# Performance work log

Hardware: AMD Instinct MI355X
Metric: run time of the kernel (lower is better)

The kernel has to match this reference:

```python
import math
import jax, jax.numpy as jnp
import numpy as np

B, T, C, H, DQK, DV = 2, 2048, 1024, 16, 64, 64


def setup_inputs() -> dict:
    key = jax.random.key(0)
    ks = jax.random.split(key, 5)
    x = jax.random.normal(ks[0], (B, T, C), dtype=jnp.float32)
    # randw: randn(*d) / sqrt(d[-1])
    w_q = jax.random.normal(ks[1], (H, DQK, C), dtype=jnp.float32) / math.sqrt(C)
    w_k = jax.random.normal(ks[2], (H, DQK, C), dtype=jnp.float32) / math.sqrt(C)
    w_v = jax.random.normal(ks[3], (H, DV, C), dtype=jnp.float32) / math.sqrt(C)
    w_o = jax.random.normal(ks[4], (DV * H, C), dtype=jnp.float32) / math.sqrt(C)
    return {"x": x, "w_q": w_q, "w_k": w_k, "w_v": w_v, "w_o": w_o}


def reference(x, w_q, w_k, w_v, w_o):
    # Full-sequence causal forward (bs_q.first == 0, nb == T): caches are
    # fully written in one shot, so they reduce to the plain projections.
    n, t, c = x.shape
    q = jnp.einsum('ntc,hdc->nhtd', x, w_q)
    k = jnp.einsum('ntc,hdc->nhtd', x, w_k)
    v = jnp.einsum('ntc,hdc->nhtd', x, w_v)
    scale = 1.0 / math.sqrt(w_q.shape[1])
    a = jnp.einsum('nhtd,nhsd->nhts', q, k) * scale  # [n,h,t,s]
    causal = jnp.arange(t)[:, None] < jnp.arange(t)[None, :]  # True above diag
    a = jnp.where(causal[None, None, :, :], -jnp.inf, a)
    a = jax.nn.softmax(a, axis=3)
    y = jnp.einsum('nhts,nhsd->nthd', a, v).reshape(n, t, -1)  # [n,t,h*dv]
    return y @ w_o  # cache_y, [n,t,c]
```

## Files before the change

### kernel.cpp

```cpp
#include <hip/hip_runtime.h>


typedef short bf16x4 __attribute__((ext_vector_type(4)));
typedef short bf16x8 __attribute__((ext_vector_type(8)));
typedef float f32x4 __attribute__((ext_vector_type(4)));

#define MFMA_BF16 __builtin_amdgcn_mfma_f32_16x16x32_bf16

#define QSCALE 0.18033688011112042f

__device__ __forceinline__ unsigned short f2bf(float f) {
    union { float f; unsigned u; } un; un.f = f;
    unsigned r = un.u + 0x7fffu + ((un.u >> 16) & 1u);
    return (unsigned short)(r >> 16);
}
__device__ __forceinline__ unsigned pk2(float a, float b) {
    return (unsigned)f2bf(a) | ((unsigned)f2bf(b) << 16);
}
__device__ __forceinline__ unsigned pk2t(float a, float b) {
    union { float f; unsigned u; } ua, ub; ua.f = a; ub.f = b;
    return __builtin_amdgcn_perm(ub.u, ua.u, 0x07060302u);
}
__device__ __forceinline__ void gload16(const void* g, void* l) {
    __builtin_amdgcn_global_load_lds(
        (const __attribute__((address_space(1))) unsigned int*)g,
        (__attribute__((address_space(3))) unsigned int*)l, 16, 0, 0);
}

__global__ __launch_bounds__(256) void prep(
    const float* __restrict__ x, const float* __restrict__ wq,
    const float* __restrict__ wk, const float* __restrict__ wv,
    const float* __restrict__ wo,
    unsigned short* __restrict__ x16, unsigned short* __restrict__ wq16,
    unsigned short* __restrict__ wk16, unsigned short* __restrict__ wv16,
    unsigned short* __restrict__ wot)
{
    const int bid = blockIdx.x;
    if (bid < 3584) {
        const float* s; unsigned short* d; int off;
        if (bid < 2048)      { s = x;  d = x16;  off = bid * 2048; }
        else if (bid < 2560) { s = wq; d = wq16; off = (bid - 2048) * 2048; }
        else if (bid < 3072) { s = wk; d = wk16; off = (bid - 2560) * 2048; }
        else                 { s = wv; d = wv16; off = (bid - 3072) * 2048; }
        int i = off + threadIdx.x * 8;
        float4 f0 = *(const float4*)&s[i], f1 = *(const float4*)&s[i + 4];
        uint4 o;
        o.x = pk2(f0.x, f0.y); o.y = pk2(f0.z, f0.w);
        o.z = pk2(f1.x, f1.y); o.w = pk2(f1.z, f1.w);
        *(uint4*)&d[i] = o;
    } else {
        __shared__ unsigned short t[64 * 72];
        const int b2 = bid - 3584;
        const int k0 = (b2 & 15) << 6, n0 = (b2 >> 4) << 6;
        const int r = threadIdx.x >> 2, cg = (threadIdx.x & 3) << 4;
        const float* src = &wo[(k0 + r) * 1024 + n0 + cg];
        #pragma unroll
        for (int j = 0; j < 16; j += 4) {
            float4 f = *(const float4*)&src[j];
            t[(cg + j + 0) * 72 + r] = f2bf(f.x);
            t[(cg + j + 1) * 72 + r] = f2bf(f.y);
            t[(cg + j + 2) * 72 + r] = f2bf(f.z);
            t[(cg + j + 3) * 72 + r] = f2bf(f.w);
        }
        __syncthreads();
        unsigned short* dst = &wot[(n0 + r) * 1024 + k0 + cg];
        unsigned short* tr = &t[r * 72 + cg];
        unsigned v[16];
        #pragma unroll
        for (int j = 0; j < 16; ++j) v[j] = tr[j];
        uint4 o0, o1;
        o0.x = v[0] | (v[1] << 16);   o0.y = v[2] | (v[3] << 16);
        o0.z = v[4] | (v[5] << 16);   o0.w = v[6] | (v[7] << 16);
        o1.x = v[8] | (v[9] << 16);   o1.y = v[10] | (v[11] << 16);
        o1.z = v[12] | (v[13] << 16); o1.w = v[14] | (v[15] << 16);
        *(uint4*)&dst[0] = o0;
        *(uint4*)&dst[8] = o1;
    }
}

__device__ __forceinline__ void gemm_body(
    const unsigned short* __restrict__ A, const unsigned short* __restrict__ Bm,
    void* __restrict__ C, int m0, int n0, int mode, int ldc, float sc)
{
    __shared__ unsigned short sa[2][128 * 32];
    __shared__ unsigned short sb[2][128 * 32];
    const int tid = threadIdx.x, wave = tid >> 6, lane = tid & 63;
    const int l15 = lane & 15, l4 = lane >> 4;
    const int wm = (wave >> 1) << 6, wn = (wave & 1) << 6;

    const int r16 = lane >> 2;
    const int gcol = (((lane & 3) ^ ((r16 >> 1) & 3)) << 3);
    const int rcol = (l4 ^ ((l15 >> 1) & 3)) << 3;
    const unsigned short* Ag0 = &A[(size_t)(m0 + wave * 16 + r16) * 1024 + gcol];
    const unsigned short* Ag1 = Ag0 + (size_t)64 * 1024;
    const unsigned short* Bg0 = &Bm[(size_t)(n0 + wave * 16 + r16) * 1024 + gcol];
    const unsigned short* Bg1 = Bg0 + (size_t)64 * 1024;
    const int lb0 = (wave * 16) * 32;
    const int lb1 = (64 + wave * 16) * 32;

    gload16(Ag0, &sa[0][lb0]);
    gload16(Ag1, &sa[0][lb1]);
    gload16(Bg0, &sb[0][lb0]);
    gload16(Bg1, &sb[0][lb1]);
    __syncthreads();

    f32x4 acc[4][4] = {};

    #pragma unroll
    for (int kk = 0; kk < 32; ++kk) {
        const int cur = kk & 1;
        if (kk < 31) {
            const int off = (kk + 1) * 32;
            const int nxt = 1 - cur;
            gload16(Ag0 + off, &sa[nxt][lb0]);
            gload16(Ag1 + off, &sa[nxt][lb1]);
            gload16(Bg0 + off, &sb[nxt][lb0]);
            gload16(Bg1 + off, &sb[nxt][lb1]);
        }
        bf16x8 af[4], bf4[4];
        #pragma unroll
        for (int i = 0; i < 4; ++i)
            af[i] = *(const bf16x8*)&sa[cur][(wm + i * 16 + l15) * 32 + rcol];
        #pragma unroll
        for (int j = 0; j < 4; ++j)
            bf4[j] = *(const bf16x8*)&sb[cur][(wn + j * 16 + l15) * 32 + rcol];
        #pragma unroll
        for (int i = 0; i < 4; ++i)
            #pragma unroll
            for (int j = 0; j < 4; ++j)
                acc[i][j] = MFMA_BF16(af[i], bf4[j], acc[i][j], 0, 0, 0);
        __syncthreads();
    }

    #pragma unroll
    for (int i = 0; i < 4; ++i)
        #pragma unroll
        for (int j = 0; j < 4; ++j)
            #pragma unroll
            for (int r = 0; r < 4; ++r) {
                int row = m0 + wm + i * 16 + l4 * 4 + r;
                int col = n0 + wn + j * 16 + l15;
                float val = acc[i][j][r];
                if (mode == 0) {
                    int nb = row >> 11, t = row & 2047;
                    int hh = col >> 6, dd = col & 63;
                    ((unsigned short*)C)[(((nb << 4) + hh) * 2048 + t) * 64 + dd] =
                        f2bf(val * sc);
                } else if (mode == 1) {
                    ((float*)C)[(size_t)row * ldc + col] = val;
                } else {
                    int s = col & 31;
                    int cp = (col & ~31) | (((s >> 2) & 3) << 3)
                                         | (((s >> 4) & 1) << 2) | (s & 3);
                    ((unsigned short*)C)[(size_t)row * ldc + cp] = f2bf(val);
                }
            }
}

__global__ __launch_bounds__(256) void proj(
    const unsigned short* __restrict__ x16,
    const unsigned short* __restrict__ wq16,
    const unsigned short* __restrict__ wk16,
    const unsigned short* __restrict__ wv16,
    unsigned short* __restrict__ qbuf,
    unsigned short* __restrict__ kbuf,
    unsigned short* __restrict__ vtb)
{
    const int bid = blockIdx.x;
    if (bid < 512) {
        int m0 = (bid & 31) << 7;
        int n0g = (bid >> 5) << 7;
        if (n0g < 1024)
            gemm_body(x16, wq16, qbuf, m0, n0g, 0, 0, QSCALE);
        else
            gemm_body(x16, wk16, kbuf, m0, n0g - 1024, 0, 0, 1.0f);
    } else {
        int v = bid - 512;
        gemm_body(wv16, x16, vtb, (v & 7) << 7, (v >> 3) << 7, 2, 4096, 1.0f);
    }
}

__global__ __launch_bounds__(256) void outp(
    const unsigned short* __restrict__ ybuf,
    const unsigned short* __restrict__ wot,
    float* __restrict__ out)
{
    const int bid = blockIdx.x;
    gemm_body(ybuf, wot, out, (bid & 31) << 7, (bid >> 5) << 7, 1, 1024, 1.0f);
}

__global__ __launch_bounds__(512, 2) void attn(
    const unsigned short* __restrict__ q,
    const unsigned short* __restrict__ k,
    const unsigned short* __restrict__ vt,
    unsigned short* __restrict__ y)
{
    __shared__ unsigned short sk[2][2][64 * 64];
    __shared__ unsigned short sv[2][2][64 * 64];
    const int tid = threadIdx.x, wave = tid >> 6, lane = tid & 63;
    const int ws = wave & 3, wk2 = wave >> 2;
    const int l15 = lane & 15, l4 = lane >> 4;
    const int bid = blockIdx.x;
    const int pr = bid >> 5;
    const int bh = bid & 31;
    const int nb = bh >> 4, hh = bh & 15;
    const size_t base = (size_t)bh << 17;

    const int lrow = lane >> 3;
    const int gch = ((lane & 7) ^ lrow) << 3;
    const int row = wave * 8 + lrow;
    const unsigned short* kg = &k[base + (size_t)row * 64 + gch];
    const unsigned short* vg = &vt[(size_t)((hh << 6) + row) * 4096 + (nb << 11) + gch];
    const int lb = (wave * 8) * 64;

    const int rch0 = ((0 + l4) ^ (l15 & 7)) << 3;
    const int rch1 = ((4 + l4) ^ (l15 & 7)) << 3;

    float* mrg = (float*)&sk[0][0][0];
    float* lsr = (float*)&sv[0][0][0];
    const int mslot = (ws << 6) + lane;
    const int mb = mslot << 5;

    auto process = [&](const int t) {
        const int q0 = t << 7;
        bf16x8 qf[2][2];
        #pragma unroll
        for (int g = 0; g < 2; ++g)
            #pragma unroll
            for (int ks = 0; ks < 2; ++ks)
                qf[g][ks] = *(const bf16x8*)
                    &q[base + (size_t)(q0 + (g << 6) + ws * 16 + l15) * 64 + ks * 32 + l4 * 8];

        float l_sum[2] = {0.f, 0.f};
        f32x4 acc[2][4] = {};
        const int nsup = t + 1;

        auto stage_pair = [&](const int sbuf, const int p) {
            gload16(kg + ((size_t)p << 13),        &sk[sbuf][0][lb]);
            gload16(kg + ((size_t)p << 13) + 4096, &sk[sbuf][1][lb]);
            gload16(vg + (p << 7),      &sv[sbuf][0][lb]);
            gload16(vg + (p << 7) + 64, &sv[sbuf][1][lb]);
        };

        stage_pair(0, 0);
        __syncthreads();

        auto sstep = [&](const int cur, const int p) {
            if (p + 1 < nsup) stage_pair(cur ^ 1, p + 1);
            const int st = 2 * p + wk2;
            const unsigned short* skc = &sk[cur][wk2][0];
            const unsigned short* svc = &sv[cur][wk2][0];

            f32x4 s_acc[2][4] = {};
            #pragma unroll
            for (int ns = 0; ns < 4; ++ns) {
                bf16x8 kf0 = *(const bf16x8*)&skc[(ns * 16 + l15) * 64 + rch0];
                bf16x8 kf1 = *(const bf16x8*)&skc[(ns * 16 + l15) * 64 + rch1];
                s_acc[0][ns] = MFMA_BF16(kf0, qf[0][0], s_acc[0][ns], 0, 0, 0);
                s_acc[0][ns] = MFMA_BF16(kf1, qf[0][1], s_acc[0][ns], 0, 0, 0);
                s_acc[1][ns] = MFMA_BF16(kf0, qf[1][0], s_acc[1][ns], 0, 0, 0);
                s_acc[1][ns] = MFMA_BF16(kf1, qf[1][1], s_acc[1][ns], 0, 0, 0);
            }

            if (p == nsup - 1) {
                const int sb = st << 6;
                #pragma unroll
                for (int g = 0; g < 2; ++g) {
                    const int qlg = q0 + (g << 6) + ws * 16 + l15;
                    #pragma unroll
                    for (int ns = 0; ns < 4; ++ns)
                        #pragma unroll
                        for (int r = 0; r < 4; ++r)
                            if (sb + ns * 16 + l4 * 4 + r > qlg) s_acc[g][ns][r] = -1e30f;
                }
            }

            float pe[2][4][4];
            #pragma unroll
            for (int g = 0; g < 2; ++g)
                #pragma unroll
                for (int ns = 0; ns < 4; ++ns) {
                    #pragma unroll
                    for (int r = 0; r < 4; ++r) pe[g][ns][r] = exp2f(s_acc[g][ns][r]);
                    l_sum[g] += (pe[g][ns][0] + pe[g][ns][1]) + (pe[g][ns][2] + pe[g][ns][3]);
                }

            #pragma unroll
            for (int ks = 0; ks < 2; ++ks) {
                bf16x8 pf0, pf1;
                {
                    uint4 pw;
                    pw.x = pk2t(pe[0][2 * ks][0], pe[0][2 * ks][1]);
                    pw.y = pk2t(pe[0][2 * ks][2], pe[0][2 * ks][3]);
                    pw.z = pk2t(pe[0][2 * ks + 1][0], pe[0][2 * ks + 1][1]);
                    pw.w = pk2t(pe[0][2 * ks + 1][2], pe[0][2 * ks + 1][3]);
                    pf0 = *(bf16x8*)&pw;
                }
                {
                    uint4 pw;
                    pw.x = pk2t(pe[1][2 * ks][0], pe[1][2 * ks][1]);
                    pw.y = pk2t(pe[1][2 * ks][2], pe[1][2 * ks][3]);
                    pw.z = pk2t(pe[1][2 * ks + 1][0], pe[1][2 * ks + 1][1]);
                    pw.w = pk2t(pe[1][2 * ks + 1][2], pe[1][2 * ks + 1][3]);
                    pf1 = *(bf16x8*)&pw;
                }
                const int rch = ks ? rch1 : rch0;
                #pragma unroll
                for (int ds = 0; ds < 4; ++ds) {
                    bf16x8 vf = *(const bf16x8*)&svc[(ds * 16 + l15) * 64 + rch];
                    acc[0][ds] = MFMA_BF16(vf, pf0, acc[0][ds], 0, 0, 0);
                    acc[1][ds] = MFMA_BF16(vf, pf1, acc[1][ds], 0, 0, 0);
                }
            }
            __syncthreads();
        };

        int p = 0;
        for (; p + 2 <= nsup; p += 2) { sstep(0, p); sstep(1, p + 1); }
        if (p < nsup) sstep(0, p);

        if (wk2 == 1) {
            #pragma unroll
            for (int g = 0; g < 2; ++g)
                #pragma unroll
                for (int ds = 0; ds < 4; ++ds) {
                    const int c = g * 4 + ds;
                    *(f32x4*)&mrg[mb + ((c ^ (lane & 7)) << 2)] = acc[g][ds];
                }
            lsr[(mslot << 1) + 0] = l_sum[0];
            lsr[(mslot << 1) + 1] = l_sum[1];
        }
        __syncthreads();
        if (wk2 == 0) {
            #pragma unroll
            for (int g = 0; g < 2; ++g)
                #pragma unroll
                for (int ds = 0; ds < 4; ++ds) {
                    const int c = g * 4 + ds;
                    acc[g][ds] += *(const f32x4*)&mrg[mb + ((c ^ (lane & 7)) << 2)];
                }
            l_sum[0] += lsr[(mslot << 1) + 0];
            l_sum[1] += lsr[(mslot << 1) + 1];

            #pragma unroll
            for (int g = 0; g < 2; ++g) {
                float ls = l_sum[g];
                ls += __shfl_xor(ls, 16);
                ls += __shfl_xor(ls, 32);
                const float rl = __builtin_amdgcn_rcpf(ls);

                const size_t rowbase =
                    ((size_t)((nb << 11) + q0 + (g << 6) + ws * 16 + l15) << 10) + (hh << 6) + l4 * 4;
                #pragma unroll
                for (int ds = 0; ds < 4; ++ds) {
                    uint2 o;
                    o.x = pk2(acc[g][ds][0] * rl, acc[g][ds][1] * rl);
                    o.y = pk2(acc[g][ds][2] * rl, acc[g][ds][3] * rl);
                    *(uint2*)&y[rowbase + ds * 16] = o;
                }
            }
        }
        __syncthreads();
    };

    process(15 - pr);
    process(pr);
}

extern "C" void kernel_launch(void* const* d_in, const int* in_sizes, int n_in,
                              void* d_out, int out_size, void* d_ws, size_t ws_size,
                              hipStream_t stream) {
    const float* x  = (const float*)d_in[0];
    const float* wq = (const float*)d_in[1];
    const float* wk = (const float*)d_in[2];
    const float* wv = (const float*)d_in[3];
    const float* wo = (const float*)d_in[4];
    float* out = (float*)d_out;

    const size_t M1 = 1u << 20;
    unsigned short* x16  = (unsigned short*)d_ws;
    unsigned short* wq16 = x16 + 4 * M1;
    unsigned short* wk16 = wq16 + M1;
    unsigned short* wv16 = wk16 + M1;
    unsigned short* wot  = wv16 + M1;
    unsigned short* qbuf = wot + M1;
    unsigned short* kbuf = qbuf + 4 * M1;
    unsigned short* vtb  = kbuf + 4 * M1;
    unsigned short* ybuf = vtb + 4 * M1;

    dim3 blk(256);
    prep<<<3840, blk, 0, stream>>>(x, wq, wk, wv, wo, x16, wq16, wk16, wv16, wot);
    proj<<<768, blk, 0, stream>>>(x16, wq16, wk16, wv16, qbuf, kbuf, vtb);
    attn<<<256, dim3(512), 0, stream>>>(qbuf, kbuf, vtb, ybuf);
    outp<<<256, blk, 0, stream>>>(ybuf, wot, out);
}
```

Measured before the change: 169.2 us.

## Split-K the output projection with atomics and raise MFMA priority in attention

The output projection now runs as 512 blocks, each covering half of the K dimension, so the 256 CUs are better filled. Partial sums go to the output through float atomic adds, and the prep kernel gains 512 extra blocks that zero the output first. Separately, the attention kernel raises wave priority around its MFMA sections with s_setprio. The cost is atomic traffic on the output plus an extra zeroing write pass, and float atomic ordering may make results nondeterministic.

Result: slower. 199.7 us (+18.0%).

```diff
diff --git a/kernel.cpp b/kernel.cpp
--- a/kernel.cpp
+++ b/kernel.cpp
@@ -33,7 +33,7 @@
     const float* __restrict__ wo,
     unsigned short* __restrict__ x16, unsigned short* __restrict__ wq16,
     unsigned short* __restrict__ wk16, unsigned short* __restrict__ wv16,
-    unsigned short* __restrict__ wot)
+    unsigned short* __restrict__ wot, float* __restrict__ outz)
 {
     const int bid = blockIdx.x;
     if (bid < 3584) {
@@ -48,7 +48,7 @@
         o.x = pk2(f0.x, f0.y); o.y = pk2(f0.z, f0.w);
         o.z = pk2(f1.x, f1.y); o.w = pk2(f1.z, f1.w);
         *(uint4*)&d[i] = o;
-    } else {
+    } else if (bid < 3840) {
         __shared__ unsigned short t[64 * 72];
         const int b2 = bid - 3584;
         const int k0 = (b2 & 15) << 6, n0 = (b2 >> 4) << 6;
@@ -75,12 +75,18 @@
         o1.z = v[12] | (v[13] << 16); o1.w = v[14] | (v[15] << 16);
         *(uint4*)&dst[0] = o0;
         *(uint4*)&dst[8] = o1;
+    } else {
+        float4 z = make_float4(0.f, 0.f, 0.f, 0.f);
+        float* d = &outz[(size_t)(bid - 3840) * 8192 + threadIdx.x * 4];
+        #pragma unroll
+        for (int j = 0; j < 8; ++j) *(float4*)&d[j * 1024] = z;
     }
 }
 
+template<int MODE, int KCNT>
 __device__ __forceinline__ void gemm_body(
     const unsigned short* __restrict__ A, const unsigned short* __restrict__ Bm,
-    void* __restrict__ C, int m0, int n0, int mode, int ldc, float sc)
+    void* __restrict__ C, int m0, int n0, int ldc, float sc, int kbase)
 {
     __shared__ unsigned short sa[2][128 * 32];
     __shared__ unsigned short sb[2][128 * 32];
@@ -91,9 +97,9 @@
     const int r16 = lane >> 2;
     const int gcol = (((lane & 3) ^ ((r16 >> 1) & 3)) << 3);
     const int rcol = (l4 ^ ((l15 >> 1) & 3)) << 3;
-    const unsigned short* Ag0 = &A[(size_t)(m0 + wave * 16 + r16) * 1024 + gcol];
+    const unsigned short* Ag0 = &A[(size_t)(m0 + wave * 16 + r16) * 1024 + kbase + gcol];
     const unsigned short* Ag1 = Ag0 + (size_t)64 * 1024;
-    const unsigned short* Bg0 = &Bm[(size_t)(n0 + wave * 16 + r16) * 1024 + gcol];
+    const unsigned short* Bg0 = &Bm[(size_t)(n0 + wave * 16 + r16) * 1024 + kbase + gcol];
     const unsigned short* Bg1 = Bg0 + (size_t)64 * 1024;
     const int lb0 = (wave * 16) * 32;
     const int lb1 = (64 + wave * 16) * 32;
@@ -107,9 +113,9 @@
     f32x4 acc[4][4] = {};
 
     #pragma unroll
-    for (int kk = 0; kk < 32; ++kk) {
+    for (int kk = 0; kk < KCNT; ++kk) {
         const int cur = kk & 1;
-        if (kk < 31) {
+        if (kk < KCNT - 1) {
             const int off = (kk + 1) * 32;
             const int nxt = 1 - cur;
             gload16(Ag0 + off, &sa[nxt][lb0]);
@@ -141,18 +147,20 @@
                 int row = m0 + wm + i * 16 + l4 * 4 + r;
                 int col = n0 + wn + j * 16 + l15;
                 float val = acc[i][j][r];
-                if (mode == 0) {
+                if (MODE == 0) {
                     int nb = row >> 11, t = row & 2047;
                     int hh = col >> 6, dd = col & 63;
                     ((unsigned short*)C)[(((nb << 4) + hh) * 2048 + t) * 64 + dd] =
                         f2bf(val * sc);
-                } else if (mode == 1) {
+                } else if (MODE == 1) {
                     ((float*)C)[(size_t)row * ldc + col] = val;
-                } else {
+                } else if (MODE == 2) {
                     int s = col & 31;
                     int cp = (col & ~31) | (((s >> 2) & 3) << 3)
                                          | (((s >> 4) & 1) << 2) | (s & 3);
                     ((unsigned short*)C)[(size_t)row * ldc + cp] = f2bf(val);
+                } else {
+                    unsafeAtomicAdd(&((float*)C)[(size_t)row * ldc + col], val);
                 }
             }
 }
@@ -171,12 +179,12 @@
         int m0 = (bid & 31) << 7;
         int n0g = (bid >> 5) << 7;
         if (n0g < 1024)
-            gemm_body(x16, wq16, qbuf, m0, n0g, 0, 0, QSCALE);
+            gemm_body<0, 32>(x16, wq16, qbuf, m0, n0g, 0, QSCALE, 0);
         else
-            gemm_body(x16, wk16, kbuf, m0, n0g - 1024, 0, 0, 1.0f);
+            gemm_body<0, 32>(x16, wk16, kbuf, m0, n0g - 1024, 0, 1.0f, 0);
     } else {
         int v = bid - 512;
-        gemm_body(wv16, x16, vtb, (v & 7) << 7, (v >> 3) << 7, 2, 4096, 1.0f);
+        gemm_body<2, 32>(wv16, x16, vtb, (v & 7) << 7, (v >> 3) << 7, 4096, 1.0f, 0);
     }
 }
 
@@ -186,7 +194,10 @@
     float* __restrict__ out)
 {
     const int bid = blockIdx.x;
-    gemm_body(ybuf, wot, out, (bid & 31) << 7, (bid >> 5) << 7, 1, 1024, 1.0f);
+    const int kh = bid >> 8;
+    const int b2 = bid & 255;
+    gemm_body<3, 16>(ybuf, wot, out, (b2 & 31) << 7, (b2 >> 5) << 7,
+                     1024, 1.0f, kh << 9);
 }
 
 __global__ __launch_bounds__(512, 2) void attn(
@@ -252,6 +263,7 @@
             const unsigned short* svc = &sv[cur][wk2][0];
 
             f32x4 s_acc[2][4] = {};
+            __builtin_amdgcn_s_setprio(1);
             #pragma unroll
             for (int ns = 0; ns < 4; ++ns) {
                 bf16x8 kf0 = *(const bf16x8*)&skc[(ns * 16 + l15) * 64 + rch0];
@@ -261,6 +273,7 @@
                 s_acc[1][ns] = MFMA_BF16(kf0, qf[1][0], s_acc[1][ns], 0, 0, 0);
                 s_acc[1][ns] = MFMA_BF16(kf1, qf[1][1], s_acc[1][ns], 0, 0, 0);
             }
+            __builtin_amdgcn_s_setprio(0);
 
             if (p == nsup - 1) {
                 const int sb = st << 6;
@@ -305,12 +318,14 @@
                     pf1 = *(bf16x8*)&pw;
                 }
                 const int rch = ks ? rch1 : rch0;
+                __builtin_amdgcn_s_setprio(1);
                 #pragma unroll
                 for (int ds = 0; ds < 4; ++ds) {
                     bf16x8 vf = *(const bf16x8*)&svc[(ds * 16 + l15) * 64 + rch];
                     acc[0][ds] = MFMA_BF16(vf, pf0, acc[0][ds], 0, 0, 0);
                     acc[1][ds] = MFMA_BF16(vf, pf1, acc[1][ds], 0, 0, 0);
                 }
+                __builtin_amdgcn_s_setprio(0);
             }
             __syncthreads();
         };
@@ -389,8 +404,8 @@
     unsigned short* ybuf = vtb + 4 * M1;
 
     dim3 blk(256);
-    prep<<<3840, blk, 0, stream>>>(x, wq, wk, wv, wo, x16, wq16, wk16, wv16, wot);
+    prep<<<4352, blk, 0, stream>>>(x, wq, wk, wv, wo, x16, wq16, wk16, wv16, wot, out);
     proj<<<768, blk, 0, stream>>>(x16, wq16, wk16, wv16, qbuf, kbuf, vtb);
     attn<<<256, dim3(512), 0, stream>>>(qbuf, kbuf, vtb, ybuf);
-    outp<<<256, blk, 0, stream>>>(ybuf, wot, out);
-}
+    outp<<<512, blk, 0, stream>>>(ybuf, wot, out);
+}
```
